# Performance work log

Hardware: AMD Instinct MI355X
Metric: run time of the kernel (lower is better)

## Reference

```python
import jax, jax.numpy as jnp
import numpy as np

R = 2
TAU = 0.1
EPS = 1e-7

# normalized 3x3 Sobel kernels (kornia SpatialGradient, normalized=True -> /8)
_GX = jnp.array([[-1., 0., 1.], [-2., 0., 2.], [-1., 0., 1.]], dtype=jnp.float32) / 8.0
_GY = _GX.T

K = 2 * R - 1  # 3
_HORIZ = jnp.zeros((K, K), jnp.float32).at[R - 1, :].set(1.0)
_VERT = jnp.zeros((K, K), jnp.float32).at[:, R - 1].set(1.0)
_LEAD = jnp.eye(K, dtype=jnp.float32)
_CNT = jnp.fliplr(jnp.eye(K, dtype=jnp.float32))


def _conv2d_same(x, k2d, mode):
    # depthwise 'same' cross-correlation, x: (B,C,H,W), k2d: (k,k)
    C = x.shape[1]
    p = k2d.shape[-1] // 2
    xp = jnp.pad(x, ((0, 0), (0, 0), (p, p), (p, p)), mode=mode)
    kern = jnp.broadcast_to(k2d[None, None], (C, 1) + k2d.shape)
    return jax.lax.conv_general_dilated(
        xp, kern, (1, 1), 'VALID',
        dimension_numbers=('NCHW', 'OIHW', 'NCHW'),
        feature_group_count=C)


def _grad_angles(t):
    # kornia SpatialGradient pads with replicate ('edge')
    gx = _conv2d_same(t, _GX, 'edge')
    gy = _conv2d_same(t, _GY, 'edge')
    grad_xx = _conv2d_same(gx, _GX, 'edge')
    grad_xy = _conv2d_same(gy, _GX, 'edge')
    grad_yy = _conv2d_same(gy, _GY, 'edge')
    theta = jnp.arctan(grad_yy * jnp.sign(-grad_xy + EPS) / (grad_xx + EPS))
    angle = theta * (180.0 / np.pi)
    return jnp.where(angle < 0, angle + 180.0, angle)


def _nms_loss(true_labels, pred_labels):
    angle = _grad_angles(true_labels)
    mask = (true_labels > 0).astype(jnp.float32)

    th_h = mask * (((angle >= 0) & (angle < 22.5)) | ((angle >= 157.5) & (angle < 180))).astype(jnp.float32)
    th_cd = mask * ((angle >= 22.5) & (angle < 67.5)).astype(jnp.float32)
    th_v = mask * ((angle >= 67.5) & (angle < 112.5)).astype(jnp.float32)
    th_ld = mask * ((angle > 112.5) & (angle < 157.5)).astype(jnp.float32)

    e = jnp.exp(pred_labels * TAU)

    def term(th, kern):
        f = _conv2d_same(e, kern, 'reflect')  # kornia filter2D default border 'reflect'
        return th * jnp.log(jnp.clip(e / (f + EPS), EPS, 1.0))

    total = (term(th_h, _HORIZ) + term(th_v, _VERT) +
             term(th_ld, _LEAD) + term(th_cd, _CNT))
    # sum over (C,H,W) per sample, mean over batch, negate
    return -jnp.mean(jnp.sum(total, axis=(1, 2, 3)))


def setup_inputs() -> dict:
    key = jax.random.key(0)
    k1, k2 = jax.random.split(key)
    B, C, H, W = 4, 19, 512, 512
    true_labels = jax.random.normal(k1, (B, C, H, W), dtype=jnp.float32)
    pred_labels = jax.random.normal(k2, (B, C, H, W), dtype=jnp.float32)
    return {"true_labels": true_labels, "pred_labels": pred_labels}


def reference(true_labels, pred_labels):
    return _nms_loss(true_labels, pred_labels)
```

## Files before the change

### kernel.cpp

```cpp
#include <hip/hip_runtime.h>

#define BAND 16
#define NITER (BAND + 4)
#define NSLOT 1024

__global__ __launch_bounds__(64) void nms_loss_kernel(
    const float* __restrict__ tl, const float* __restrict__ pl,
    double* __restrict__ acc_d, float* __restrict__ acc_f,
    int H, int W)
{
    const int y0   = blockIdx.x * BAND;
    const int slab = blockIdx.y;
    const int ch   = blockIdx.z;
    const float* tc = tl + (size_t)ch * H * W;
    const float* pc = pl + (size_t)ch * H * W;
    const int tid = threadIdx.x;
    const int c0  = (slab << 8) + (tid << 2);
    const int oa  = max(c0 - 4, 0);
    const int oc  = min(c0 + 4, W - 4);
    const bool eL = (c0 == 0), eR = (c0 == W - 4);
    const float eL2 = eL ? 2.f : 0.f, eR2 = eR ? 2.f : 0.f;

    float P1h[5][4], P2h[5][4], P3h[5][4];
    float eh[3][6], tch[3][4];
    float t12[12], p12[12];

    #define LOADROW(I) {                                                            \
        int tr_ = y0 - 2 + (I); tr_ = min(max(tr_, 0), H - 1);                       \
        int pr_ = y0 - 3 + (I); pr_ = pr_ < 0 ? -pr_ : (pr_ >= H ? 2*H-2-pr_ : pr_); \
        const float* tb_ = tc + (size_t)tr_ * W;                                     \
        const float* pb_ = pc + (size_t)pr_ * W;                                     \
        float4 a_ = *(const float4*)(tb_ + oa);                                      \
        float4 b_ = *(const float4*)(tb_ + c0);                                      \
        float4 c_ = *(const float4*)(tb_ + oc);                                      \
        t12[2]=a_.z; t12[3]=a_.w;                                                    \
        t12[4]=b_.x; t12[5]=b_.y; t12[6]=b_.z; t12[7]=b_.w;                          \
        t12[8]=c_.x; t12[9]=c_.y;                                                    \
        a_ = *(const float4*)(pb_ + oa);                                             \
        b_ = *(const float4*)(pb_ + c0);                                             \
        c_ = *(const float4*)(pb_ + oc);                                             \
        p12[3]=a_.w;                                                                 \
        p12[4]=b_.x; p12[5]=b_.y; p12[6]=b_.z; p12[7]=b_.w;                          \
        p12[8]=c_.x;                                                                 \
        t12[2] = eL ? t12[5] : t12[2];                             \
        t12[3] = eL ? t12[4] : t12[3];                             \
        t12[8] = eR ? t12[7] : t12[8];                        \
        t12[9] = eR ? t12[6] : t12[9];                        \
        p12[3] = eL ? p12[5] : p12[3];                      \
        p12[8] = eR ? p12[6] : p12[8]; }

    LOADROW(0)

    float partial = 0.f;

    #pragma unroll
    for (int i = 0; i < NITER; ++i) {
        const int sP = i % 5, sE = i % 3;

        #pragma unroll
        for (int j = 0; j < 4; ++j) {
            float a0 = t12[j+2], a1 = t12[j+3], a2 = t12[j+4], a3 = t12[j+5], a4 = t12[j+6];
            float s04 = a0 + a4, s13 = a1 + a3;
            P1h[sP][j] = fmaf(-2.f, a2, s04);
            P3h[sP][j] = fmaf(6.f, a2, fmaf(4.f, s13, s04));
            P2h[sP][j] = fmaf(2.f, a3 - a1, a4 - a0);
            tch[sE][j] = a2;
        }
        P1h[sP][0] = fmaf(eL2, t12[4] - t12[5], P1h[sP][0]);
        P1h[sP][3] = fmaf(eR2, t12[7] - t12[6], P1h[sP][3]);
        #pragma unroll
        for (int m = 0; m < 6; ++m) eh[sE][m] = __expf(0.1f * p12[m+3]);

        if (i + 1 < NITER) LOADROW(i + 1)

        if (i >= 4) {
            const int y = y0 + i - 4;
            const int s0=(i-4)%5, s1=(i-3)%5, s2=(i-2)%5, s3=(i-1)%5, s4=i%5;
            const int et=(i-2)%3, em=(i-1)%3, eb=i%3;
            const bool ytop = (y == 0), ybot = (y == H - 1);
            #pragma unroll
            for (int j = 0; j < 4; ++j) {
                float a04 = P1h[s0][j] + P1h[s4][j], a13 = P1h[s1][j] + P1h[s3][j];
                float xx = fmaf(6.f, P1h[s2][j], fmaf(4.f, a13, a04));
                float xy = fmaf(2.f, P2h[s3][j] - P2h[s1][j], P2h[s4][j] - P2h[s0][j]);
                float yy = fmaf(-2.f, P3h[s2][j], P3h[s0][j] + P3h[s4][j]);
                if (ytop) {
                    xx += P1h[s3][j] - P1h[s2][j];
                    xy += P2h[s3][j] - P2h[s2][j];
                    yy += P3h[s2][j] - P3h[s3][j];
                } else if (ybot) {
                    xx += P1h[s1][j] - P1h[s2][j];
                    xy += P2h[s2][j] - P2h[s1][j];
                    yy += P3h[s2][j] - P3h[s1][j];
                }
                if (tch[et][j] > 0.f) {
                    float den = xx + 6.4e-6f;
                    float sa  = 6.4e-6f - xy;
                    float ax = fabsf(den), ay = fabsf(yy);
                    bool isH = ay < 0.41421356f * ax;
                    bool isV = ay >= 2.41421356f * ax;
                    bool qp  = ((yy * sa) * den) > 0.f;
                    float ec = eh[em][j + 1];
                    float n1 = isH ? eh[em][j + 2] : (isV ? eh[eb][j + 1] : (qp ? eh[eb][j] : eh[eb][j + 2]));
                    float n2 = isH ? eh[em][j]     : (isV ? eh[et][j + 1] : (qp ? eh[et][j + 2] : eh[et][j]));
                    partial += __logf(__fdividef(ec, ec + n1 + n2 + 1e-7f));
                }
            }
        }
    }

    for (int off = 32; off > 0; off >>= 1)
        partial += __shfl_down(partial, off, 64);
    if (tid == 0) {
        int fid = (blockIdx.z * gridDim.y + blockIdx.y) * gridDim.x + blockIdx.x;
        if (acc_d) atomicAdd(&acc_d[fid & (NSLOT - 1)], (double)partial);
        else       atomicAdd(acc_f, partial);
    }
}

__global__ void finalize_kernel(const double* acc_d, float* out,
                                int use_double, float inv_b)
{
    if (use_double) {
        int l = threadIdx.x;
        double s = 0.0;
        for (int i = l; i < NSLOT; i += 64) s += acc_d[i];
        for (int off = 32; off > 0; off >>= 1) s += __shfl_down(s, off, 64);
        if (l == 0) out[0] = (float)(-s * (double)inv_b);
    } else {
        if (threadIdx.x == 0) out[0] = -out[0] * inv_b;
    }
}

extern "C" void kernel_launch(void* const* d_in, const int* in_sizes, int n_in,
                              void* d_out, int out_size, void* d_ws, size_t ws_size,
                              hipStream_t stream)
{
    const float* tl = (const float*)d_in[0];
    const float* pl = (const float*)d_in[1];
    float* out = (float*)d_out;

    const int H = 512, W = 512, B = 4;

    double* acc_d = nullptr;
    float* acc_f = nullptr;
    int use_double = 0;
    if (ws_size >= NSLOT * sizeof(double)) {
        acc_d = (double*)d_ws;
        use_double = 1;
        hipMemsetAsync(acc_d, 0, NSLOT * sizeof(double), stream);
    } else {
        acc_f = out;
        hipMemsetAsync(out, 0, sizeof(float), stream);
    }

    dim3 grid(H / BAND, W / 256, 76);
    nms_loss_kernel<<<grid, 64, 0, stream>>>(tl, pl, acc_d, acc_f, H, W);
    finalize_kernel<<<1, 64, 0, stream>>>(acc_d, out, use_double, 1.0f / (float)B);
}
```

Baseline: 60.56 us.

## Stage input bands into LDS with direct global-to-LDS loads

```diff
diff --git a/kernel.cpp b/kernel.cpp
--- a/kernel.cpp
+++ b/kernel.cpp
@@ -3,45 +3,77 @@
 #define BAND 16
 #define NITER (BAND + 4)
 #define NSLOT 1024
+#define SLABW 256
 
 __global__ __launch_bounds__(64) void nms_loss_kernel(
     const float* __restrict__ tl, const float* __restrict__ pl,
     double* __restrict__ acc_d, float* __restrict__ acc_f,
     int H, int W)
 {
+    __shared__ __align__(16) float t_s[20][264];
+    __shared__ __align__(16) float p_s[18][264];
+
     const int y0   = blockIdx.x * BAND;
     const int slab = blockIdx.y;
     const int ch   = blockIdx.z;
+    const int slabc = slab << 8;
+    const int nslab = W / SLABW;
     const float* tc = tl + (size_t)ch * H * W;
     const float* pc = pl + (size_t)ch * H * W;
     const int tid = threadIdx.x;
-    const int c0  = (slab << 8) + (tid << 2);
-    const int oa  = max(c0 - 4, 0);
-    const int oc  = min(c0 + 4, W - 4);
+    const int c0  = slabc + (tid << 2);
     const bool eL = (c0 == 0), eR = (c0 == W - 4);
     const float eL2 = eL ? 2.f : 0.f, eR2 = eR ? 2.f : 0.f;
+    const bool hl = (tid == 0) && (slab > 0);
+    const bool hr = (tid == 63) && (slab < nslab - 1);
+    const bool hseam = hl || hr;
+    const int hcol = hl ? (slabc - 2) : (slabc + SLABW);
+
+    for (int rr = 0; rr < 20; ++rr) {
+        int tr = min(max(y0 - 2 + rr, 0), H - 1);
+        const float* ga = tc + (size_t)tr * W + slabc + (tid << 2);
+        __builtin_amdgcn_global_load_lds(
+            (const __attribute__((address_space(1))) void*)ga,
+            (__attribute__((address_space(3))) void*)&t_s[rr][4], 16, 0, 0);
+    }
+    for (int rr = 0; rr < 18; ++rr) {
+        int pr = y0 - 1 + rr; pr = pr < 0 ? -pr : (pr >= H ? 2 * H - 2 - pr : pr);
+        const float* ga = pc + (size_t)pr * W + slabc + (tid << 2);
+        __builtin_amdgcn_global_load_lds(
+            (const __attribute__((address_space(1))) void*)ga,
+            (__attribute__((address_space(3))) void*)&p_s[rr][4], 16, 0, 0);
+    }
+    asm volatile("s_waitcnt vmcnt(0)" ::: "memory");
+    __builtin_amdgcn_sched_barrier(0);
 
     float P1h[5][4], P2h[5][4], P3h[5][4];
     float eh[3][6], tch[3][4];
     float t12[12], p12[12];
 
     #define LOADROW(I) {                                                            \
-        int tr_ = y0 - 2 + (I); tr_ = min(max(tr_, 0), H - 1);                       \
-        int pr_ = y0 - 3 + (I); pr_ = pr_ < 0 ? -pr_ : (pr_ >= H ? 2*H-2-pr_ : pr_); \
-        const float* tb_ = tc + (size_t)tr_ * W;                                     \
-        const float* pb_ = pc + (size_t)pr_ * W;                                     \
-        float4 a_ = *(const float4*)(tb_ + oa);                                      \
-        float4 b_ = *(const float4*)(tb_ + c0);                                      \
-        float4 c_ = *(const float4*)(tb_ + oc);                                      \
-        t12[2]=a_.z; t12[3]=a_.w;                                                    \
-        t12[4]=b_.x; t12[5]=b_.y; t12[6]=b_.z; t12[7]=b_.w;                          \
-        t12[8]=c_.x; t12[9]=c_.y;                                                    \
-        a_ = *(const float4*)(pb_ + oa);                                             \
-        b_ = *(const float4*)(pb_ + c0);                                             \
-        c_ = *(const float4*)(pb_ + oc);                                             \
-        p12[3]=a_.w;                                                                 \
-        p12[4]=b_.x; p12[5]=b_.y; p12[6]=b_.z; p12[7]=b_.w;                          \
-        p12[8]=c_.x;                                                                 \
+        const float* trow = &t_s[(I)][(tid << 2) + 2];                               \
+        float2 q0 = *(const float2*)(trow);                                          \
+        float2 q1 = *(const float2*)(trow + 2);                                      \
+        float2 q2 = *(const float2*)(trow + 4);                                      \
+        float2 q3 = *(const float2*)(trow + 6);                                      \
+        t12[2]=q0.x; t12[3]=q0.y; t12[4]=q1.x; t12[5]=q1.y;                          \
+        t12[6]=q2.x; t12[7]=q2.y; t12[8]=q3.x; t12[9]=q3.y;                          \
+        const int prr = (I) >= 2 ? (I) - 2 : 0;                                      \
+        const float* prow = &p_s[prr][(tid << 2) + 2];                               \
+        q0 = *(const float2*)(prow);                                                 \
+        q1 = *(const float2*)(prow + 2);                                             \
+        q2 = *(const float2*)(prow + 4);                                             \
+        q3 = *(const float2*)(prow + 6);                                             \
+        p12[2]=q0.x; p12[3]=q0.y; p12[4]=q1.x; p12[5]=q1.y;                          \
+        p12[6]=q2.x; p12[7]=q2.y; p12[8]=q3.x; p12[9]=q3.y;                          \
+        if (hseam) {                                                                 \
+            int tr_ = min(max(y0 - 2 + (I), 0), H - 1);                              \
+            float2 th_ = *(const float2*)(tc + (size_t)tr_ * W + hcol);              \
+            int pr_ = y0 - 1 + prr; pr_ = pr_ < 0 ? -pr_ : (pr_ >= H ? 2*H-2-pr_ : pr_); \
+            float2 ph_ = *(const float2*)(pc + (size_t)pr_ * W + hcol);              \
+            if (hl) { t12[2]=th_.x; t12[3]=th_.y; p12[3]=ph_.y; }                    \
+            else    { t12[8]=th_.x; t12[9]=th_.y; p12[8]=ph_.x; }                    \
+        }                                                                            \
         t12[2] = eL ? t12[5] : t12[2];                             \
         t12[3] = eL ? t12[4] : t12[3];                             \
         t12[8] = eR ? t12[7] : t12[8];                        \
@@ -154,7 +186,7 @@
         hipMemsetAsync(out, 0, sizeof(float), stream);
     }
 
-    dim3 grid(H / BAND, W / 256, 76);
+    dim3 grid(H / BAND, W / SLABW, 76);
     nms_loss_kernel<<<grid, 64, 0, stream>>>(tl, pl, acc_d, acc_f, H, W);
     finalize_kernel<<<1, 64, 0, stream>>>(acc_d, out, use_double, 1.0f / (float)B);
 }
```

Measured after the change: 121.6 us. 101% more time.
